# Kernel tuning notes

Measured on AMD Instinct MI355X. Metric: run time of the kernel, lower is better.

Reference implementation:

```python
import jax, jax.numpy as jnp
import numpy as np

N_HEADS = 8
HEAD_D = 64


def setup_inputs() -> dict:
    key = jax.random.key(0)
    ks = jax.random.split(key, 7)
    b, ds, dc = 4, 4096, 256
    ls, lc = 512, 512
    inner = N_HEADS * HEAD_D  # 512
    out_dim = 512
    data = jax.random.normal(ks[0], (b, ds, dc), dtype=jnp.float32)
    latent = jax.random.normal(ks[1], (b, ls, lc), dtype=jnp.float32)
    # torch nn.Linear weights are [out_features, in_features]
    Wq = jax.random.normal(ks[2], (inner, lc), dtype=jnp.float32) * (lc ** -0.5)
    Wk = jax.random.normal(ks[3], (inner, dc), dtype=jnp.float32) * (dc ** -0.5)
    Wv = jax.random.normal(ks[4], (inner, dc), dtype=jnp.float32) * (dc ** -0.5)
    Wo = jax.random.normal(ks[5], (out_dim, inner), dtype=jnp.float32) * (inner ** -0.5)
    bo = jax.random.normal(ks[6], (out_dim,), dtype=jnp.float32) * 0.02
    return {"data": data, "latent": latent, "Wq": Wq, "Wk": Wk, "Wv": Wv, "Wo": Wo, "bo": bo}


def reference(data, latent, Wq, Wk, Wv, Wo, bo):
    b, ds, _ = data.shape
    ls = latent.shape[1]
    scale = HEAD_D ** -0.5
    # projections, split into heads
    Q = (latent @ Wq.T).reshape(b, ls, N_HEADS, HEAD_D)  # [b,ls,h,d]
    K = (data @ Wk.T).reshape(b, ds, N_HEADS, HEAD_D)    # [b,ds,h,d]
    V = (data @ Wv.T).reshape(b, ds, N_HEADS, HEAD_D)
    # logits [b, ds, ls, h]; original broadcasts then sums over head_d -> einsum
    logits = jnp.einsum('blhd,bshd->bslh', Q, K) * scale
    # softmax over key axis (dim 1 = ds), matching attn_logits.softmax(1)
    attn = jax.nn.softmax(logits, axis=1)
    # weighted sum over keys: [b, ls, h, d] -> [b, ls, inner]
    out = jnp.einsum('bshd,bslh->blhd', V, attn).reshape(b, ls, N_HEADS * HEAD_D)
    # output Linear (dropout is identity in eval)
    return out @ Wo.T + bo
```

## Files before the change

### kernel.cpp

```cpp
#include <hip/hip_runtime.h>

typedef __bf16 bf16;
typedef __bf16 bf16x8 __attribute__((ext_vector_type(8)));
typedef float  f32x4  __attribute__((ext_vector_type(4)));


__device__ __forceinline__ bf16x8 cvt8(float4 a, float4 b) {
    bf16x8 r;
    r[0] = (bf16)a.x; r[1] = (bf16)a.y; r[2] = (bf16)a.z; r[3] = (bf16)a.w;
    r[4] = (bf16)b.x; r[5] = (bf16)b.y; r[6] = (bf16)b.z; r[7] = (bf16)b.w;
    return r;
}

#define LDT 136
__global__ __launch_bounds__(256) void proj_kvq(
    const float* __restrict__ data, const float* __restrict__ latent,
    const float* __restrict__ Wk, const float* __restrict__ Wv, const float* __restrict__ Wq,
    bf16* __restrict__ K_b, bf16* __restrict__ Vt_b, bf16* __restrict__ Q_b)
{
    __shared__ __align__(16) bf16 arena[128 * LDT];
    bf16* As = arena;
    bf16* Bs = arena + 4096;

    const int bx = blockIdx.x;
    const float* A; const float* Bm; bf16* outb;
    int Kdim, mode, m0, n0;
    if (bx < 512)       { A = data;   Bm = Wk; outb = K_b;  Kdim = 256; mode = 0; m0 = (bx & 127) * 128;         n0 = (bx >> 7) * 128; }
    else if (bx < 1024) { int t = bx - 512;  A = data;   Bm = Wv; outb = Vt_b; Kdim = 256; mode = 1; m0 = (t & 127) * 128; n0 = (t >> 7) * 128; }
    else                { int t = bx - 1024; A = latent; Bm = Wq; outb = Q_b;  Kdim = 512; mode = 2; m0 = (t & 15) * 128;  n0 = (t >> 4) * 128; }

    const int tid = threadIdx.x;
    const int wave = tid >> 6, lane = tid & 63;
    const int wm = wave >> 1, wn = wave & 1;
    const int l15 = lane & 15, quad = lane >> 4;
    const int rowA = tid >> 2;
    const int c8 = (tid & 3) * 8;

    const float* Arow0 = A + (size_t)(m0 + rowA) * Kdim + c8;
    const float* Arow1 = A + (size_t)(m0 + 64 + rowA) * Kdim + c8;
    const float* Brow0 = Bm + (size_t)(n0 + rowA) * Kdim + c8;
    const float* Brow1 = Bm + (size_t)(n0 + 64 + rowA) * Kdim + c8;

    f32x4 acc[4][4] = {};
    float4 a00, a01, a10, a11, b00, b01, b10, b11;

#define LOADP(k) do { \
        a00 = *(const float4*)(Arow0 + (k));  a01 = *(const float4*)(Arow0 + (k) + 4); \
        a10 = *(const float4*)(Arow1 + (k));  a11 = *(const float4*)(Arow1 + (k) + 4); \
        b00 = *(const float4*)(Brow0 + (k));  b01 = *(const float4*)(Brow0 + (k) + 4); \
        b10 = *(const float4*)(Brow1 + (k));  b11 = *(const float4*)(Brow1 + (k) + 4); \
    } while (0)

    LOADP(0);

    for (int k0 = 0; k0 < Kdim; k0 += 32) {
        __syncthreads();
        *(bf16x8*)(As + (size_t)tid * 8)        = cvt8(a00, a01);
        *(bf16x8*)(As + 2048 + (size_t)tid * 8) = cvt8(a10, a11);
        *(bf16x8*)(Bs + (size_t)tid * 8)        = cvt8(b00, b01);
        *(bf16x8*)(Bs + 2048 + (size_t)tid * 8) = cvt8(b10, b11);
        if (k0 + 32 < Kdim) LOADP(k0 + 32);
        __syncthreads();

        bf16x8 af[4], bfr[4];
        #pragma unroll
        for (int mt = 0; mt < 4; mt++)
            af[mt] = *(const bf16x8*)(As + (wm * 64 + mt * 16 + l15) * 32 + quad * 8);
        #pragma unroll
        for (int nt = 0; nt < 4; nt++)
            bfr[nt] = *(const bf16x8*)(Bs + (wn * 64 + nt * 16 + l15) * 32 + quad * 8);
        #pragma unroll
        for (int mt = 0; mt < 4; mt++)
            #pragma unroll
            for (int nt = 0; nt < 4; nt++)
                acc[mt][nt] = __builtin_amdgcn_mfma_f32_16x16x32_bf16(af[mt], bfr[nt], acc[mt][nt], 0, 0, 0);
    }
#undef LOADP

    __syncthreads();
    #pragma unroll
    for (int mt = 0; mt < 4; mt++) {
        #pragma unroll
        for (int nt = 0; nt < 4; nt++) {
            #pragma unroll
            for (int r = 0; r < 4; r++) {
                int ml = wm * 64 + mt * 16 + quad * 4 + r;
                int nl = wn * 64 + nt * 16 + l15;
                bf16 v = (bf16)acc[mt][nt][r];
                if (mode == 1) arena[nl * LDT + ml] = v;
                else           arena[ml * LDT + nl] = v;
            }
        }
    }
    __syncthreads();

    #pragma unroll
    for (int c = 0; c < 8; c++) {
        int idx = c * 256 + tid;
        int row = idx >> 4, col = (idx & 15) * 8;
        bf16x8 vv = *(const bf16x8*)(arena + row * LDT + col);
        if (mode == 0) {
            int m = m0 + row, n = n0 + col;
            *(bf16x8*)(outb + (size_t)((m >> 12) * 8 + (n >> 6)) * 262144 + (m & 4095) * 64 + (n & 63)) = vv;
        } else if (mode == 1) {
            int d = n0 + row, s = m0 + col;
            *(bf16x8*)(outb + (size_t)((s >> 12) * 8 + (d >> 6)) * 262144 + (d & 63) * 4096 + (s & 4095)) = vv;
        } else {
            int m = m0 + row, n = n0 + col;
            *(bf16x8*)(outb + (size_t)((m >> 9) * 8 + (n >> 6)) * 32768 + (m & 511) * 64 + (n & 63)) = vv;
        }
    }
}

#define LDK 72
__global__ __launch_bounds__(256) void flash_attn(
    const bf16* __restrict__ Q, const bf16* __restrict__ K,
    const bf16* __restrict__ Vt, float* __restrict__ Opart, float* __restrict__ lbuf)
{
    __shared__ bf16 Ks[64 * LDK];
    __shared__ bf16 Vs[64 * LDK];
    __shared__ bf16 Ps[4][16 * LDK];

    const int tid = threadIdx.x;
    const int bx = blockIdx.x;
    const int qt = bx >> 7;
    const int bh = (bx & 127) >> 2;
    const int ks = bx & 3;
    const int wave = tid >> 6, lane = tid & 63;
    const int l15 = lane & 15, quad = lane >> 4;

    const bf16* Qb = Q + (size_t)bh * 32768 + (size_t)(qt * 64 + wave * 16 + l15) * 64;
    bf16x8 aq[2];
    aq[0] = *(const bf16x8*)(Qb + quad * 8);
    aq[1] = *(const bf16x8*)(Qb + 32 + quad * 8);

    const bf16* Kb = K + (size_t)bh * 262144;
    const bf16* Vb = Vt + (size_t)bh * 262144;

    f32x4 oacc[4] = {};
    float lpart[4] = {0.f, 0.f, 0.f, 0.f};
    const float scale = 0.125f;

    const int i0 = tid, i1 = tid + 256;
    const int r0 = i0 >> 3, c0 = (i0 & 7) * 8;
    const int r1 = i1 >> 3, c1 = (i1 & 7) * 8;

    const int kstart = ks * 1024, kend = kstart + 1024;

    uint4 pk0 = *(const uint4*)(Kb + (size_t)(kstart + r0) * 64 + c0);
    uint4 pk1 = *(const uint4*)(Kb + (size_t)(kstart + r1) * 64 + c1);
    uint4 pv0 = *(const uint4*)(Vb + (size_t)r0 * 4096 + kstart + c0);
    uint4 pv1 = *(const uint4*)(Vb + (size_t)r1 * 4096 + kstart + c1);

    for (int key0 = kstart; key0 < kend; key0 += 64) {
        __syncthreads();
        *(uint4*)(Ks + r0 * LDK + c0) = pk0;
        *(uint4*)(Ks + r1 * LDK + c1) = pk1;
        *(uint4*)(Vs + r0 * LDK + c0) = pv0;
        *(uint4*)(Vs + r1 * LDK + c1) = pv1;
        if (key0 + 64 < kend) {
            pk0 = *(const uint4*)(Kb + (size_t)(key0 + 64 + r0) * 64 + c0);
            pk1 = *(const uint4*)(Kb + (size_t)(key0 + 64 + r1) * 64 + c1);
            pv0 = *(const uint4*)(Vb + (size_t)r0 * 4096 + key0 + 64 + c0);
            pv1 = *(const uint4*)(Vb + (size_t)r1 * 4096 + key0 + 64 + c1);
        }
        __syncthreads();

        float p[4][4];
        #pragma unroll
        for (int nt = 0; nt < 4; nt++) {
            f32x4 z = {};
            #pragma unroll
            for (int kf = 0; kf < 2; kf++) {
                bf16x8 bk = *(const bf16x8*)(Ks + (nt * 16 + l15) * LDK + kf * 32 + quad * 8);
                z = __builtin_amdgcn_mfma_f32_16x16x32_bf16(aq[kf], bk, z, 0, 0, 0);
            }
            #pragma unroll
            for (int r = 0; r < 4; r++) {
                float e = __expf(z[r] * scale);
                p[r][nt] = e;
                lpart[r] += e;
            }
        }

        #pragma unroll
        for (int r = 0; r < 4; r++)
            #pragma unroll
            for (int nt = 0; nt < 4; nt++)
                Ps[wave][(quad * 4 + r) * LDK + nt * 16 + l15] = (bf16)p[r][nt];

        bf16x8 ap[2];
        ap[0] = *(const bf16x8*)(&Ps[wave][l15 * LDK + quad * 8]);
        ap[1] = *(const bf16x8*)(&Ps[wave][l15 * LDK + 32 + quad * 8]);
        #pragma unroll
        for (int dt = 0; dt < 4; dt++) {
            #pragma unroll
            for (int kf = 0; kf < 2; kf++) {
                bf16x8 bv = *(const bf16x8*)(Vs + (dt * 16 + l15) * LDK + kf * 32 + quad * 8);
                oacc[dt] = __builtin_amdgcn_mfma_f32_16x16x32_bf16(ap[kf], bv, oacc[dt], 0, 0, 0);
            }
        }
    }

    #pragma unroll
    for (int r = 0; r < 4; r++) {
        #pragma unroll
        for (int off = 1; off < 16; off <<= 1) lpart[r] += __shfl_xor(lpart[r], off, 64);
    }

    const int rowbase = bh * 512 + qt * 64 + wave * 16 + quad * 4;
    #pragma unroll
    for (int dt = 0; dt < 4; dt++) {
        #pragma unroll
        for (int r = 0; r < 4; r++) {
            Opart[((size_t)ks * 16384 + rowbase + r) * 64 + dt * 16 + l15] = oacc[dt][r];
        }
    }
    if (l15 == 0) {
        #pragma unroll
        for (int r = 0; r < 4; r++)
            lbuf[(size_t)ks * 16384 + rowbase + r] = lpart[r];
    }
}

__global__ __launch_bounds__(256) void gemm_out(
    const float* __restrict__ Opart, const float* __restrict__ lbuf,
    const float* __restrict__ Wo, const float* __restrict__ bo, float* __restrict__ out)
{
    __shared__ bf16 As[64 * 32];
    __shared__ bf16 Bs[64 * 32];
    const int tid = threadIdx.x;
    const int m0 = blockIdx.x * 64, n0 = blockIdx.y * 64;
    const int wave = tid >> 6, lane = tid & 63;
    const int wm = wave >> 1, wn = wave & 1;
    const int l15 = lane & 15, quad = lane >> 4;
    const int rowA = tid >> 2;
    const int c8 = (tid & 3) * 8;
    const int m = m0 + rowA;
    const int mhi = (m >> 9) << 3, mlo = m & 511;

    f32x4 acc[2][2] = {};
    float4 pa[8]; float pl[4]; float4 pb0, pb1;

    auto loadA = [&](int k0) {
        int kc = k0 + c8;
        int arow = (mhi + (kc >> 6)) * 512 + mlo;
        int d0 = kc & 63;
        #pragma unroll
        for (int ks = 0; ks < 4; ks++) {
            pl[ks] = lbuf[(size_t)ks * 16384 + arow];
            pa[2 * ks]     = *(const float4*)(Opart + ((size_t)ks * 16384 + arow) * 64 + d0);
            pa[2 * ks + 1] = *(const float4*)(Opart + ((size_t)ks * 16384 + arow) * 64 + d0 + 4);
        }
    };
    auto loadB = [&](int k0) {
        pb0 = *(const float4*)(Wo + (size_t)(n0 + rowA) * 512 + k0 + c8);
        pb1 = *(const float4*)(Wo + (size_t)(n0 + rowA) * 512 + k0 + c8 + 4);
    };

    loadA(0); loadB(0);

    for (int k0 = 0; k0 < 512; k0 += 32) {
        __syncthreads();
        {
            float L = pl[0] + pl[1] + pl[2] + pl[3];
            float inv = 1.0f / L;
            float4 s0, s1;
            s0.x = pa[0].x + pa[2].x + pa[4].x + pa[6].x;
            s0.y = pa[0].y + pa[2].y + pa[4].y + pa[6].y;
            s0.z = pa[0].z + pa[2].z + pa[4].z + pa[6].z;
            s0.w = pa[0].w + pa[2].w + pa[4].w + pa[6].w;
            s1.x = pa[1].x + pa[3].x + pa[5].x + pa[7].x;
            s1.y = pa[1].y + pa[3].y + pa[5].y + pa[7].y;
            s1.z = pa[1].z + pa[3].z + pa[5].z + pa[7].z;
            s1.w = pa[1].w + pa[3].w + pa[5].w + pa[7].w;
            s0.x *= inv; s0.y *= inv; s0.z *= inv; s0.w *= inv;
            s1.x *= inv; s1.y *= inv; s1.z *= inv; s1.w *= inv;
            *(bf16x8*)(As + (size_t)tid * 8) = cvt8(s0, s1);
            *(bf16x8*)(Bs + (size_t)tid * 8) = cvt8(pb0, pb1);
        }
        if (k0 + 32 < 512) { loadA(k0 + 32); loadB(k0 + 32); }
        __syncthreads();

        bf16x8 af[2], bfr[2];
        #pragma unroll
        for (int mt = 0; mt < 2; mt++)
            af[mt] = *(const bf16x8*)(As + (wm * 32 + mt * 16 + l15) * 32 + quad * 8);
        #pragma unroll
        for (int nt = 0; nt < 2; nt++)
            bfr[nt] = *(const bf16x8*)(Bs + (wn * 32 + nt * 16 + l15) * 32 + quad * 8);
        #pragma unroll
        for (int mt = 0; mt < 2; mt++)
            #pragma unroll
            for (int nt = 0; nt < 2; nt++)
                acc[mt][nt] = __builtin_amdgcn_mfma_f32_16x16x32_bf16(af[mt], bfr[nt], acc[mt][nt], 0, 0, 0);
    }

    #pragma unroll
    for (int mt = 0; mt < 2; mt++) {
        #pragma unroll
        for (int nt = 0; nt < 2; nt++) {
            #pragma unroll
            for (int r = 0; r < 4; r++) {
                int mm = m0 + wm * 32 + mt * 16 + quad * 4 + r;
                int nn = n0 + wn * 32 + nt * 16 + l15;
                out[(size_t)mm * 512 + nn] = acc[mt][nt][r] + bo[nn];
            }
        }
    }
}

extern "C" void kernel_launch(void* const* d_in, const int* in_sizes, int n_in,
                              void* d_out, int out_size, void* d_ws, size_t ws_size,
                              hipStream_t stream) {
    const float* data   = (const float*)d_in[0];
    const float* latent = (const float*)d_in[1];
    const float* Wq = (const float*)d_in[2];
    const float* Wk = (const float*)d_in[3];
    const float* Wv = (const float*)d_in[4];
    const float* Wo = (const float*)d_in[5];
    const float* bo = (const float*)d_in[6];
    float* out = (float*)d_out;

    bf16* ws = (bf16*)d_ws;
    bf16* Q_b    = ws;
    bf16* K_b    = Q_b + 1048576;
    bf16* Vt_b   = K_b + 8388608;
    float* Opart = (float*)(Vt_b + 8388608);
    float* lbuf  = Opart + 4 * 16384 * 64;

    proj_kvq<<<1088, 256, 0, stream>>>(data, latent, Wk, Wv, Wq, K_b, Vt_b, Q_b);
    flash_attn<<<1024, 256, 0, stream>>>(Q_b, K_b, Vt_b, Opart, lbuf);
    gemm_out<<<dim3(32, 8), 256, 0, stream>>>(Opart, lbuf, Wo, bo, out);
}
```

Before: 157.8 us.

## Fuse projection, attention and output GEMM into one persistent kernel with grid barriers

Replaces the three kernel launches with a single persistent kernel of 512 blocks. Blocks pull projection tiles from an atomic work queue, then pass through software grid barriers before running attention and then the output GEMM. Each attention block now handles two query tiles, so loaded K/V tiles are reused across more queries. The aim is to cut launch gaps and tail effects. The cost is spin-wait barriers, a memset launch, and a deadlock risk if not all 512 blocks are co-resident.

```diff
diff --git a/kernel.cpp b/kernel.cpp
--- a/kernel.cpp
+++ b/kernel.cpp
@@ -4,6 +4,9 @@
 typedef __bf16 bf16x8 __attribute__((ext_vector_type(8)));
 typedef float  f32x4  __attribute__((ext_vector_type(4)));
 
+#define LDT 136
+#define LDK 72
+#define NBLK 512
 
 __device__ __forceinline__ bf16x8 cvt8(float4 a, float4 b) {
     bf16x8 r;
@@ -12,22 +15,31 @@
     return r;
 }
 
-#define LDT 136
-__global__ __launch_bounds__(256) void proj_kvq(
+__device__ __forceinline__ void gridbar(unsigned* c, unsigned n) {
+    __syncthreads();
+    __threadfence();
+    if (threadIdx.x == 0) {
+        __hip_atomic_fetch_add(c, 1u, __ATOMIC_ACQ_REL, __HIP_MEMORY_SCOPE_AGENT);
+        while (__hip_atomic_load(c, __ATOMIC_ACQUIRE, __HIP_MEMORY_SCOPE_AGENT) < n) {
+            __builtin_amdgcn_s_sleep(2);
+        }
+    }
+    __syncthreads();
+    __threadfence();
+}
+
+__device__ void proj_task(int t,
     const float* __restrict__ data, const float* __restrict__ latent,
     const float* __restrict__ Wk, const float* __restrict__ Wv, const float* __restrict__ Wq,
-    bf16* __restrict__ K_b, bf16* __restrict__ Vt_b, bf16* __restrict__ Q_b)
+    bf16* __restrict__ K_b, bf16* __restrict__ Vt_b, bf16* __restrict__ Q_b, bf16* arena)
 {
-    __shared__ __align__(16) bf16 arena[128 * LDT];
     bf16* As = arena;
     bf16* Bs = arena + 4096;
-
-    const int bx = blockIdx.x;
     const float* A; const float* Bm; bf16* outb;
     int Kdim, mode, m0, n0;
-    if (bx < 512)       { A = data;   Bm = Wk; outb = K_b;  Kdim = 256; mode = 0; m0 = (bx & 127) * 128;         n0 = (bx >> 7) * 128; }
-    else if (bx < 1024) { int t = bx - 512;  A = data;   Bm = Wv; outb = Vt_b; Kdim = 256; mode = 1; m0 = (t & 127) * 128; n0 = (t >> 7) * 128; }
-    else                { int t = bx - 1024; A = latent; Bm = Wq; outb = Q_b;  Kdim = 512; mode = 2; m0 = (t & 15) * 128;  n0 = (t >> 4) * 128; }
+    if (t < 64)       { A = latent; Bm = Wq; outb = Q_b;  Kdim = 512; mode = 2; m0 = (t & 15) * 128;  n0 = (t >> 4) * 128; }
+    else if (t < 576) { int tt = t - 64;  A = data; Bm = Wk; outb = K_b;  Kdim = 256; mode = 0; m0 = (tt & 127) * 128; n0 = (tt >> 7) * 128; }
+    else              { int tt = t - 576; A = data; Bm = Wv; outb = Vt_b; Kdim = 256; mode = 1; m0 = (tt & 127) * 128; n0 = (tt >> 7) * 128; }
 
     const int tid = threadIdx.x;
     const int wave = tid >> 6, lane = tid & 63;
@@ -52,7 +64,6 @@
     } while (0)
 
     LOADP(0);
-
     for (int k0 = 0; k0 < Kdim; k0 += 32) {
         __syncthreads();
         *(bf16x8*)(As + (size_t)tid * 8)        = cvt8(a00, a01);
@@ -112,39 +123,35 @@
     }
 }
 
-#define LDK 72
-__global__ __launch_bounds__(256) void flash_attn(
-    const bf16* __restrict__ Q, const bf16* __restrict__ K,
-    const bf16* __restrict__ Vt, float* __restrict__ Opart, float* __restrict__ lbuf)
+__device__ void flash_task(int bx,
+    const bf16* __restrict__ Q, const bf16* __restrict__ K, const bf16* __restrict__ Vt,
+    float* __restrict__ Opart, float* __restrict__ lbuf, bf16* arena)
 {
-    __shared__ bf16 Ks[64 * LDK];
-    __shared__ bf16 Vs[64 * LDK];
-    __shared__ bf16 Ps[4][16 * LDK];
+    bf16* Ks = arena;
+    bf16* Vs = arena + 64 * LDK;
+    bf16* Ps = arena + 128 * LDK;
 
     const int tid = threadIdx.x;
-    const int bx = blockIdx.x;
-    const int qt = bx >> 7;
-    const int bh = (bx & 127) >> 2;
-    const int ks = bx & 3;
+    const int qp = bx >> 7, bh = (bx >> 2) & 31, ks = bx & 3;
     const int wave = tid >> 6, lane = tid & 63;
     const int l15 = lane & 15, quad = lane >> 4;
 
-    const bf16* Qb = Q + (size_t)bh * 32768 + (size_t)(qt * 64 + wave * 16 + l15) * 64;
-    bf16x8 aq[2];
-    aq[0] = *(const bf16x8*)(Qb + quad * 8);
-    aq[1] = *(const bf16x8*)(Qb + 32 + quad * 8);
-
+    bf16x8 aq[2][2];
+    #pragma unroll
+    for (int qs = 0; qs < 2; qs++) {
+        const bf16* Qb = Q + (size_t)bh * 32768 + (size_t)((qp + qs * 4) * 64 + wave * 16 + l15) * 64;
+        aq[qs][0] = *(const bf16x8*)(Qb + quad * 8);
+        aq[qs][1] = *(const bf16x8*)(Qb + 32 + quad * 8);
+    }
     const bf16* Kb = K + (size_t)bh * 262144;
     const bf16* Vb = Vt + (size_t)bh * 262144;
 
-    f32x4 oacc[4] = {};
-    float lpart[4] = {0.f, 0.f, 0.f, 0.f};
+    f32x4 oacc[2][4] = {};
+    float lpart[2][4] = {};
     const float scale = 0.125f;
 
-    const int i0 = tid, i1 = tid + 256;
-    const int r0 = i0 >> 3, c0 = (i0 & 7) * 8;
-    const int r1 = i1 >> 3, c1 = (i1 & 7) * 8;
-
+    const int r0 = tid >> 3, c0 = (tid & 7) * 8;
+    const int r1 = (tid + 256) >> 3, c1 = ((tid + 256) & 7) * 8;
     const int kstart = ks * 1024, kend = kstart + 1024;
 
     uint4 pk0 = *(const uint4*)(Kb + (size_t)(kstart + r0) * 64 + c0);
@@ -166,71 +173,76 @@
         }
         __syncthreads();
 
-        float p[4][4];
-        #pragma unroll
-        for (int nt = 0; nt < 4; nt++) {
-            f32x4 z = {};
-            #pragma unroll
-            for (int kf = 0; kf < 2; kf++) {
-                bf16x8 bk = *(const bf16x8*)(Ks + (nt * 16 + l15) * LDK + kf * 32 + quad * 8);
-                z = __builtin_amdgcn_mfma_f32_16x16x32_bf16(aq[kf], bk, z, 0, 0, 0);
+        #pragma unroll
+        for (int qs = 0; qs < 2; qs++) {
+            float p[4][4];
+            #pragma unroll
+            for (int nt = 0; nt < 4; nt++) {
+                f32x4 z = {};
+                #pragma unroll
+                for (int kf = 0; kf < 2; kf++) {
+                    bf16x8 bk = *(const bf16x8*)(Ks + (nt * 16 + l15) * LDK + kf * 32 + quad * 8);
+                    z = __builtin_amdgcn_mfma_f32_16x16x32_bf16(aq[qs][kf], bk, z, 0, 0, 0);
+                }
+                #pragma unroll
+                for (int r = 0; r < 4; r++) {
+                    float e = __expf(z[r] * scale);
+                    p[r][nt] = e;
+                    lpart[qs][r] += e;
+                }
             }
             #pragma unroll
-            for (int r = 0; r < 4; r++) {
-                float e = __expf(z[r] * scale);
-                p[r][nt] = e;
-                lpart[r] += e;
+            for (int r = 0; r < 4; r++)
+                #pragma unroll
+                for (int nt = 0; nt < 4; nt++)
+                    Ps[wave * 16 * LDK + (quad * 4 + r) * LDK + nt * 16 + l15] = (bf16)p[r][nt];
+
+            bf16x8 ap[2];
+            ap[0] = *(const bf16x8*)(Ps + wave * 16 * LDK + l15 * LDK + quad * 8);
+            ap[1] = *(const bf16x8*)(Ps + wave * 16 * LDK + l15 * LDK + 32 + quad * 8);
+            #pragma unroll
+            for (int dt = 0; dt < 4; dt++) {
+                #pragma unroll
+                for (int kf = 0; kf < 2; kf++) {
+                    bf16x8 bv = *(const bf16x8*)(Vs + (dt * 16 + l15) * LDK + kf * 32 + quad * 8);
+                    oacc[qs][dt] = __builtin_amdgcn_mfma_f32_16x16x32_bf16(ap[kf], bv, oacc[qs][dt], 0, 0, 0);
+                }
             }
         }
-
-        #pragma unroll
-        for (int r = 0; r < 4; r++)
-            #pragma unroll
-            for (int nt = 0; nt < 4; nt++)
-                Ps[wave][(quad * 4 + r) * LDK + nt * 16 + l15] = (bf16)p[r][nt];
-
-        bf16x8 ap[2];
-        ap[0] = *(const bf16x8*)(&Ps[wave][l15 * LDK + quad * 8]);
-        ap[1] = *(const bf16x8*)(&Ps[wave][l15 * LDK + 32 + quad * 8]);
+    }
+
+    #pragma unroll
+    for (int qs = 0; qs < 2; qs++) {
+        #pragma unroll
+        for (int r = 0; r < 4; r++) {
+            #pragma unroll
+            for (int off = 1; off < 16; off <<= 1)
+                lpart[qs][r] += __shfl_xor(lpart[qs][r], off, 64);
+        }
+        const int rowbase = bh * 512 + (qp + qs * 4) * 64 + wave * 16 + quad * 4;
         #pragma unroll
         for (int dt = 0; dt < 4; dt++) {
             #pragma unroll
-            for (int kf = 0; kf < 2; kf++) {
-                bf16x8 bv = *(const bf16x8*)(Vs + (dt * 16 + l15) * LDK + kf * 32 + quad * 8);
-                oacc[dt] = __builtin_amdgcn_mfma_f32_16x16x32_bf16(ap[kf], bv, oacc[dt], 0, 0, 0);
-            }
-        }
-    }
-
-    #pragma unroll
-    for (int r = 0; r < 4; r++) {
-        #pragma unroll
-        for (int off = 1; off < 16; off <<= 1) lpart[r] += __shfl_xor(lpart[r], off, 64);
-    }
-
-    const int rowbase = bh * 512 + qt * 64 + wave * 16 + quad * 4;
-    #pragma unroll
-    for (int dt = 0; dt < 4; dt++) {
-        #pragma unroll
-        for (int r = 0; r < 4; r++) {
-            Opart[((size_t)ks * 16384 + rowbase + r) * 64 + dt * 16 + l15] = oacc[dt][r];
-        }
-    }
-    if (l15 == 0) {
-        #pragma unroll
-        for (int r = 0; r < 4; r++)
-            lbuf[(size_t)ks * 16384 + rowbase + r] = lpart[r];
-    }
-}
-
-__global__ __launch_bounds__(256) void gemm_out(
+            for (int r = 0; r < 4; r++)
+                Opart[((size_t)ks * 16384 + rowbase + r) * 64 + dt * 16 + l15] = oacc[qs][dt][r];
+        }
+        if (l15 == 0) {
+            #pragma unroll
+            for (int r = 0; r < 4; r++)
+                lbuf[(size_t)ks * 16384 + rowbase + r] = lpart[qs][r];
+        }
+    }
+}
+
+__device__ void gemm_task(int bx,
     const float* __restrict__ Opart, const float* __restrict__ lbuf,
-    const float* __restrict__ Wo, const float* __restrict__ bo, float* __restrict__ out)
+    const float* __restrict__ Wo, const float* __restrict__ bo, float* __restrict__ out,
+    bf16* arena)
 {
-    __shared__ bf16 As[64 * 32];
-    __shared__ bf16 Bs[64 * 32];
+    bf16* As = arena;
+    bf16* Bs = arena + 2048;
     const int tid = threadIdx.x;
-    const int m0 = blockIdx.x * 64, n0 = blockIdx.y * 64;
+    const int m0 = (bx >> 3) * 64, n0 = (bx & 7) * 64;
     const int wave = tid >> 6, lane = tid & 63;
     const int wm = wave >> 1, wn = wave & 1;
     const int l15 = lane & 15, quad = lane >> 4;
@@ -310,6 +322,33 @@
     }
 }
 
+__global__ __launch_bounds__(256) void mega(
+    const float* __restrict__ data, const float* __restrict__ latent,
+    const float* __restrict__ Wq, const float* __restrict__ Wk, const float* __restrict__ Wv,
+    const float* __restrict__ Wo, const float* __restrict__ bo, float* __restrict__ out,
+    bf16* __restrict__ Q_b, bf16* __restrict__ K_b, bf16* __restrict__ Vt_b,
+    float* __restrict__ Opart, float* __restrict__ lbuf, unsigned* __restrict__ ctr)
+{
+    __shared__ __align__(16) bf16 arena[128 * LDT];
+    __shared__ int sh_task;
+    const int bx = blockIdx.x;
+
+    for (;;) {
+        __syncthreads();
+        if (threadIdx.x == 0) sh_task = (int)atomicAdd(&ctr[0], 1u);
+        __syncthreads();
+        int t = sh_task;
+        if (t >= 1088) break;
+        proj_task(t, data, latent, Wk, Wv, Wq, K_b, Vt_b, Q_b, arena);
+    }
+    gridbar(&ctr[4], NBLK);
+
+    flash_task(bx, Q_b, K_b, Vt_b, Opart, lbuf, arena);
+    gridbar(&ctr[8], NBLK);
+
+    if (bx < 256) gemm_task(bx, Opart, lbuf, Wo, bo, out, arena);
+}
+
 extern "C" void kernel_launch(void* const* d_in, const int* in_sizes, int n_in,
                               void* d_out, int out_size, void* d_ws, size_t ws_size,
                               hipStream_t stream) {
@@ -328,8 +367,9 @@
     bf16* Vt_b   = K_b + 8388608;
     float* Opart = (float*)(Vt_b + 8388608);
     float* lbuf  = Opart + 4 * 16384 * 64;
-
-    proj_kvq<<<1088, 256, 0, stream>>>(data, latent, Wk, Wv, Wq, K_b, Vt_b, Q_b);
-    flash_attn<<<1024, 256, 0, stream>>>(Q_b, K_b, Vt_b, Opart, lbuf);
-    gemm_out<<<dim3(32, 8), 256, 0, stream>>>(Opart, lbuf, Wo, bo, out);
-}
+    unsigned* ctr = (unsigned*)(lbuf + 4 * 16384);
+
+    hipMemsetAsync(ctr, 0, 64, stream);
+    mega<<<NBLK, 256, 0, stream>>>(data, latent, Wq, Wk, Wv, Wo, bo, out,
+                                   Q_b, K_b, Vt_b, Opart, lbuf, ctr);
+}
```

Result: slower. 458.2 us (+190.4%).

## Process two query tiles per flash-attention block to reuse staged K/V

Applied to the files above, without the earlier changes.

Each flash_attn block now computes two 64-row query tiles against the same staged K and V tiles, with the grid halved to 512 blocks. This halves global K/V loads and shared-memory staging per query. In exchange it doubles accumulator registers and leaves fewer blocks to fill the GPU, which may reduce latency hiding.

```diff
diff --git a/kernel.cpp b/kernel.cpp
--- a/kernel.cpp
+++ b/kernel.cpp
@@ -4,6 +4,8 @@
 typedef __bf16 bf16x8 __attribute__((ext_vector_type(8)));
 typedef float  f32x4  __attribute__((ext_vector_type(4)));
 
+#define LDT 136
+#define LDK 72
 
 __device__ __forceinline__ bf16x8 cvt8(float4 a, float4 b) {
     bf16x8 r;
@@ -12,7 +14,6 @@
     return r;
 }
 
-#define LDT 136
 __global__ __launch_bounds__(256) void proj_kvq(
     const float* __restrict__ data, const float* __restrict__ latent,
     const float* __restrict__ Wk, const float* __restrict__ Wv, const float* __restrict__ Wq,
@@ -52,7 +53,6 @@
     } while (0)
 
     LOADP(0);
-
     for (int k0 = 0; k0 < Kdim; k0 += 32) {
         __syncthreads();
         *(bf16x8*)(As + (size_t)tid * 8)        = cvt8(a00, a01);
@@ -112,10 +112,9 @@
     }
 }
 
-#define LDK 72
 __global__ __launch_bounds__(256) void flash_attn(
-    const bf16* __restrict__ Q, const bf16* __restrict__ K,
-    const bf16* __restrict__ Vt, float* __restrict__ Opart, float* __restrict__ lbuf)
+    const bf16* __restrict__ Q, const bf16* __restrict__ K, const bf16* __restrict__ Vt,
+    float* __restrict__ Opart, float* __restrict__ lbuf)
 {
     __shared__ bf16 Ks[64 * LDK];
     __shared__ bf16 Vs[64 * LDK];
@@ -123,28 +122,26 @@
 
     const int tid = threadIdx.x;
     const int bx = blockIdx.x;
-    const int qt = bx >> 7;
-    const int bh = (bx & 127) >> 2;
-    const int ks = bx & 3;
+    const int qp = bx >> 7, bh = (bx >> 2) & 31, ks = bx & 3;
     const int wave = tid >> 6, lane = tid & 63;
     const int l15 = lane & 15, quad = lane >> 4;
 
-    const bf16* Qb = Q + (size_t)bh * 32768 + (size_t)(qt * 64 + wave * 16 + l15) * 64;
-    bf16x8 aq[2];
-    aq[0] = *(const bf16x8*)(Qb + quad * 8);
-    aq[1] = *(const bf16x8*)(Qb + 32 + quad * 8);
-
+    bf16x8 aq[2][2];
+    #pragma unroll
+    for (int qs = 0; qs < 2; qs++) {
+        const bf16* Qb = Q + (size_t)bh * 32768 + (size_t)((qp + qs * 4) * 64 + wave * 16 + l15) * 64;
+        aq[qs][0] = *(const bf16x8*)(Qb + quad * 8);
+        aq[qs][1] = *(const bf16x8*)(Qb + 32 + quad * 8);
+    }
     const bf16* Kb = K + (size_t)bh * 262144;
     const bf16* Vb = Vt + (size_t)bh * 262144;
 
-    f32x4 oacc[4] = {};
-    float lpart[4] = {0.f, 0.f, 0.f, 0.f};
+    f32x4 oacc[2][4] = {};
+    float lpart[2][4] = {};
     const float scale = 0.125f;
 
-    const int i0 = tid, i1 = tid + 256;
-    const int r0 = i0 >> 3, c0 = (i0 & 7) * 8;
-    const int r1 = i1 >> 3, c1 = (i1 & 7) * 8;
-
+    const int r0 = tid >> 3, c0 = (tid & 7) * 8;
+    const int r1 = (tid + 256) >> 3, c1 = ((tid + 256) & 7) * 8;
     const int kstart = ks * 1024, kend = kstart + 1024;
 
     uint4 pk0 = *(const uint4*)(Kb + (size_t)(kstart + r0) * 64 + c0);
@@ -166,60 +163,64 @@
         }
         __syncthreads();
 
-        float p[4][4];
-        #pragma unroll
-        for (int nt = 0; nt < 4; nt++) {
-            f32x4 z = {};
-            #pragma unroll
-            for (int kf = 0; kf < 2; kf++) {
-                bf16x8 bk = *(const bf16x8*)(Ks + (nt * 16 + l15) * LDK + kf * 32 + quad * 8);
-                z = __builtin_amdgcn_mfma_f32_16x16x32_bf16(aq[kf], bk, z, 0, 0, 0);
+        #pragma unroll
+        for (int qs = 0; qs < 2; qs++) {
+            float p[4][4];
+            #pragma unroll
+            for (int nt = 0; nt < 4; nt++) {
+                f32x4 z = {};
+                #pragma unroll
+                for (int kf = 0; kf < 2; kf++) {
+                    bf16x8 bk = *(const bf16x8*)(Ks + (nt * 16 + l15) * LDK + kf * 32 + quad * 8);
+                    z = __builtin_amdgcn_mfma_f32_16x16x32_bf16(aq[qs][kf], bk, z, 0, 0, 0);
+                }
+                #pragma unroll
+                for (int r = 0; r < 4; r++) {
+                    float e = __expf(z[r] * scale);
+                    p[r][nt] = e;
+                    lpart[qs][r] += e;
+                }
             }
             #pragma unroll
-            for (int r = 0; r < 4; r++) {
-                float e = __expf(z[r] * scale);
-                p[r][nt] = e;
-                lpart[r] += e;
+            for (int r = 0; r < 4; r++)
+                #pragma unroll
+                for (int nt = 0; nt < 4; nt++)
+                    Ps[wave][(quad * 4 + r) * LDK + nt * 16 + l15] = (bf16)p[r][nt];
+
+            bf16x8 ap[2];
+            ap[0] = *(const bf16x8*)(&Ps[wave][l15 * LDK + quad * 8]);
+            ap[1] = *(const bf16x8*)(&Ps[wave][l15 * LDK + 32 + quad * 8]);
+            #pragma unroll
+            for (int dt = 0; dt < 4; dt++) {
+                #pragma unroll
+                for (int kf = 0; kf < 2; kf++) {
+                    bf16x8 bv = *(const bf16x8*)(Vs + (dt * 16 + l15) * LDK + kf * 32 + quad * 8);
+                    oacc[qs][dt] = __builtin_amdgcn_mfma_f32_16x16x32_bf16(ap[kf], bv, oacc[qs][dt], 0, 0, 0);
+                }
             }
         }
-
-        #pragma unroll
-        for (int r = 0; r < 4; r++)
-            #pragma unroll
-            for (int nt = 0; nt < 4; nt++)
-                Ps[wave][(quad * 4 + r) * LDK + nt * 16 + l15] = (bf16)p[r][nt];
-
-        bf16x8 ap[2];
-        ap[0] = *(const bf16x8*)(&Ps[wave][l15 * LDK + quad * 8]);
-        ap[1] = *(const bf16x8*)(&Ps[wave][l15 * LDK + 32 + quad * 8]);
+    }
+
+    #pragma unroll
+    for (int qs = 0; qs < 2; qs++) {
+        #pragma unroll
+        for (int r = 0; r < 4; r++) {
+            #pragma unroll
+            for (int off = 1; off < 16; off <<= 1)
+                lpart[qs][r] += __shfl_xor(lpart[qs][r], off, 64);
+        }
+        const int rowbase = bh * 512 + (qp + qs * 4) * 64 + wave * 16 + quad * 4;
         #pragma unroll
         for (int dt = 0; dt < 4; dt++) {
             #pragma unroll
-            for (int kf = 0; kf < 2; kf++) {
-                bf16x8 bv = *(const bf16x8*)(Vs + (dt * 16 + l15) * LDK + kf * 32 + quad * 8);
-                oacc[dt] = __builtin_amdgcn_mfma_f32_16x16x32_bf16(ap[kf], bv, oacc[dt], 0, 0, 0);
-            }
-        }
-    }
-
-    #pragma unroll
-    for (int r = 0; r < 4; r++) {
-        #pragma unroll
-        for (int off = 1; off < 16; off <<= 1) lpart[r] += __shfl_xor(lpart[r], off, 64);
-    }
-
-    const int rowbase = bh * 512 + qt * 64 + wave * 16 + quad * 4;
-    #pragma unroll
-    for (int dt = 0; dt < 4; dt++) {
-        #pragma unroll
-        for (int r = 0; r < 4; r++) {
-            Opart[((size_t)ks * 16384 + rowbase + r) * 64 + dt * 16 + l15] = oacc[dt][r];
-        }
-    }
-    if (l15 == 0) {
-        #pragma unroll
-        for (int r = 0; r < 4; r++)
-            lbuf[(size_t)ks * 16384 + rowbase + r] = lpart[r];
+            for (int r = 0; r < 4; r++)
+                Opart[((size_t)ks * 16384 + rowbase + r) * 64 + dt * 16 + l15] = oacc[qs][dt][r];
+        }
+        if (l15 == 0) {
+            #pragma unroll
+            for (int r = 0; r < 4; r++)
+                lbuf[(size_t)ks * 16384 + rowbase + r] = lpart[qs][r];
+        }
     }
 }
 
@@ -330,6 +331,6 @@
     float* lbuf  = Opart + 4 * 16384 * 64;
 
     proj_kvq<<<1088, 256, 0, stream>>>(data, latent, Wk, Wv, Wq, K_b, Vt_b, Q_b);
-    flash_attn<<<1024, 256, 0, stream>>>(Q_b, K_b, Vt_b, Opart, lbuf);
+    flash_attn<<<512, 256, 0, stream>>>(Q_b, K_b, Vt_b, Opart, lbuf);
     gemm_out<<<dim3(32, 8), 256, 0, stream>>>(Opart, lbuf, Wo, bo, out);
 }
```

Result: slower. 164.6 us (+4.3%).
